# Kernel tuning notes

Measured on AMD Instinct MI355X. Metric: run time of the kernel, lower is better.

## Reference

```python
import jax, jax.numpy as jnp
import numpy as np

N_NODES = 100000
N_EDGES = 1600000
IN_CH, HID_CH, OUT_CH = 256, 128, 64


def setup_inputs() -> dict:
    key = jax.random.key(0)
    k_x, k_e, k1, k2, kb1, kb2 = jax.random.split(key, 6)
    x = jax.random.normal(k_x, (N_NODES, IN_CH), dtype=jnp.float32)
    edge_index = jax.random.randint(k_e, (2, N_EDGES), 0, N_NODES, dtype=jnp.int64)
    # Glorot-style init for GCN linear weights
    W1 = jax.random.normal(k1, (IN_CH, HID_CH), dtype=jnp.float32) * (1.0 / np.sqrt(IN_CH))
    b1 = jnp.zeros((HID_CH,), dtype=jnp.float32)
    W2 = jax.random.normal(k2, (HID_CH, OUT_CH), dtype=jnp.float32) * (1.0 / np.sqrt(HID_CH))
    b2 = jnp.zeros((OUT_CH,), dtype=jnp.float32)
    return {"x": x, "edge_index": edge_index, "W1": W1, "b1": b1, "W2": W2, "b2": b2}


def _gcn_norm(edge_index, n_nodes):
    # add self loops, compute D^{-1/2} (A+I) D^{-1/2} edge weights (PyG gcn_norm)
    loop = jnp.arange(n_nodes, dtype=edge_index.dtype)
    src = jnp.concatenate([edge_index[0], loop])
    dst = jnp.concatenate([edge_index[1], loop])
    deg = jax.ops.segment_sum(jnp.ones_like(src, dtype=jnp.float32), dst, num_segments=n_nodes)
    dinv = jnp.where(deg > 0, jax.lax.rsqrt(jnp.maximum(deg, 1.0)), 0.0)
    norm = dinv[src] * dinv[dst]  # [E + N]
    return src, dst, norm


def _gcn_conv(x, W, b, src, dst, norm, n_nodes):
    h = x @ W                         # linear first (PyG GCNConv)
    msg = norm[:, None] * h[src]      # gather + normalize  [E+N, out]
    agg = jax.ops.segment_sum(msg, dst, num_segments=n_nodes)
    return agg + b


def reference(x, edge_index, W1, b1, W2, b2):
    n = x.shape[0]
    src, dst, norm = _gcn_norm(edge_index, n)
    h = jax.nn.relu(_gcn_conv(x, W1, b1, src, dst, norm, n))
    # dropout is identity in eval mode
    z = _gcn_conv(h, W2, b2, src, dst, norm, n)
    # inner-product decoder on the provided edges, with sigmoid
    e_src, e_dst = edge_index[0], edge_index[1]
    logits = jnp.sum(z[e_src] * z[e_dst], axis=-1)
    return jax.nn.sigmoid(logits)
```

## Files before the change

### kernel.cpp

```cpp
#include <hip/hip_runtime.h>
#include <math.h>

#define N_NODES 100000
#define N_EDGES 1600000
#define IN_CH 256
#define HID_CH 128
#define OUT_CH 64
#define NTILES ((N_NODES + 63) / 64)
#define NB 1024
#define NPART 256
#define EPB (N_EDGES / NPART)
#define NB_USED ((N_NODES + 127) / 128)

typedef short s16x8 __attribute__((ext_vector_type(8)));
typedef unsigned short u16x8 __attribute__((ext_vector_type(8)));
typedef float f32x4 __attribute__((ext_vector_type(4)));

__device__ __forceinline__ float bf2f(unsigned short u) {
    union { unsigned int i; float f; } v;
    v.i = ((unsigned int)u) << 16;
    return v.f;
}
__device__ __forceinline__ unsigned short f2bf(float f) {
    union { float f; unsigned int i; } v;
    v.f = f;
    unsigned int u = v.i;
    return (unsigned short)((u + 0x7FFFu + ((u >> 16) & 1u)) >> 16);
}


__global__ __launch_bounds__(256) void k_hist(const int* __restrict__ dst,
                                              int* __restrict__ ghist) {
    __shared__ int h[NB];
    int b = blockIdx.x, t = threadIdx.x;
    for (int k = t; k < NB; k += 256) h[k] = 0;
    __syncthreads();
    int e0 = b * EPB;
    for (int e = e0 + t; e < e0 + EPB; e += 256)
        atomicAdd(&h[dst[e] >> 7], 1);
    __syncthreads();
    for (int k = t; k < NB; k += 256) ghist[k * NPART + b] = h[k];
}

__global__ __launch_bounds__(256) void k_scan_cols(const int* __restrict__ ghist,
                                                   int* __restrict__ goff,
                                                   int* __restrict__ btot) {
    __shared__ int tmp[NPART];
    int k = blockIdx.x, t = threadIdx.x;
    int v = ghist[k * NPART + t];
    tmp[t] = v;
    __syncthreads();
    for (int off = 1; off < NPART; off <<= 1) {
        int u = (t >= off) ? tmp[t - off] : 0;
        __syncthreads();
        tmp[t] += u;
        __syncthreads();
    }
    goff[k * NPART + t] = tmp[t] - v;
    if (t == NPART - 1) btot[k] = tmp[t];
}

__global__ __launch_bounds__(1024) void k_scan_base(const int* __restrict__ btot,
                                                    int* __restrict__ bbase) {
    __shared__ int tmp[NB];
    int t = threadIdx.x;
    int v = btot[t];
    tmp[t] = v;
    __syncthreads();
    for (int off = 1; off < NB; off <<= 1) {
        int u = (t >= off) ? tmp[t - off] : 0;
        __syncthreads();
        tmp[t] += u;
        __syncthreads();
    }
    bbase[t] = tmp[t] - v;
    if (t == NB - 1) bbase[NB] = tmp[t];
}

__global__ __launch_bounds__(256) void k_partition(const int* __restrict__ src,
                                                   const int* __restrict__ dst,
                                                   const int* __restrict__ goff,
                                                   const int* __restrict__ bbase,
                                                   int2* __restrict__ bsorted) {
    __shared__ int cur[NB];
    int b = blockIdx.x, t = threadIdx.x;
    for (int k = t; k < NB; k += 256) cur[k] = bbase[k] + goff[k * NPART + b];
    __syncthreads();
    int e0 = b * EPB;
    for (int e = e0 + t; e < e0 + EPB; e += 256) {
        int s = src[e], d = dst[e];
        int pos = atomicAdd(&cur[d >> 7], 1);
        bsorted[pos] = make_int2(s, d);
    }
}

__global__ __launch_bounds__(256) void k_bucket_csr(const int2* __restrict__ bsorted,
                                                    const int* __restrict__ bbase,
                                                    int* __restrict__ rowoff,
                                                    float* __restrict__ dinv,
                                                    int* __restrict__ csr_src) {
    __shared__ int cnt[128];
    __shared__ int tmp[256];
    __shared__ int cur[128];
    int b = blockIdx.x, t = threadIdx.x;
    int ebeg = bbase[b], eend = bbase[b + 1];
    if (t < 128) cnt[t] = 0;
    __syncthreads();
    for (int e = ebeg + t; e < eend; e += 256)
        atomicAdd(&cnt[bsorted[e].y & 127], 1);
    __syncthreads();
    int v = (t < 128) ? cnt[t] : 0;
    tmp[t] = v;
    __syncthreads();
    for (int off = 1; off < 256; off <<= 1) {
        int u = (t >= off) ? tmp[t - off] : 0;
        __syncthreads();
        tmp[t] += u;
        __syncthreads();
    }
    if (t < 128) {
        int base = ebeg + tmp[t] - v;
        cur[t] = base;
        int node = b * 128 + t;
        if (node < N_NODES) {
            rowoff[node] = base;
            dinv[node] = rsqrtf((float)v + 1.0f);
        }
    }
    __syncthreads();
    for (int e = ebeg + t; e < eend; e += 256) {
        int2 ed = bsorted[e];
        int pos = atomicAdd(&cur[ed.y & 127], 1);
        csr_src[pos] = ed.x;
    }
}

__global__ __launch_bounds__(256) void k_cast(const float* __restrict__ x,
                                              unsigned short* __restrict__ xb) {
    const int total = N_NODES * IN_CH / 8;
    int stride = gridDim.x * 256;
    for (int i = blockIdx.x * 256 + threadIdx.x; i < total; i += stride) {
        f32x4 a = *reinterpret_cast<const f32x4*>(x + (size_t)i * 8);
        f32x4 b = *reinterpret_cast<const f32x4*>(x + (size_t)i * 8 + 4);
        u16x8 o;
        o[0] = f2bf(a[0]); o[1] = f2bf(a[1]); o[2] = f2bf(a[2]); o[3] = f2bf(a[3]);
        o[4] = f2bf(b[0]); o[5] = f2bf(b[1]); o[6] = f2bf(b[2]); o[7] = f2bf(b[3]);
        *reinterpret_cast<u16x8*>(xb + (size_t)i * 8) = o;
    }
}

__global__ void k_wt1(const float* __restrict__ W1, unsigned short* __restrict__ Wf1) {
    int u = blockIdx.x * 256 + threadIdx.x;
    int f = u >> 6, lane = u & 63;
    int kk = f >> 3, nt = f & 7;
    int l15 = lane & 15, lhi = lane >> 4;
    int n = nt * 16 + l15;
    int kbase = kk * 32 + lhi * 8;
    #pragma unroll
    for (int j = 0; j < 8; ++j)
        Wf1[(size_t)u * 8 + j] = f2bf(W1[(size_t)(kbase + j) * HID_CH + n]);
}

__global__ void k_wt2(const float* __restrict__ W2, unsigned short* __restrict__ Wf2) {
    int u = blockIdx.x * 256 + threadIdx.x;
    int f = u >> 6, lane = u & 63;
    int kk = f >> 2, nt = f & 3;
    int l15 = lane & 15, lhi = lane >> 4;
    int n = nt * 16 + l15;
    int kbase = kk * 32 + lhi * 8;
    #pragma unroll
    for (int j = 0; j < 8; ++j)
        Wf2[(size_t)u * 8 + j] = f2bf(W2[(size_t)(kbase + j) * OUT_CH + n]);
}

__global__ __launch_bounds__(256, 4) void k_gemm1(const unsigned short* __restrict__ xb,
                                                  const unsigned short* __restrict__ Wf1,
                                                  const float* __restrict__ dinv,
                                                  unsigned short* __restrict__ hs1) {
    int tid = threadIdx.x;
    int w = tid >> 6;
    int lane = tid & 63;
    int l15 = lane & 15;
    int lhi = lane >> 4;
    int m0 = blockIdx.x * 64;

    int arow = m0 + w * 16 + l15;
    int arowc = (arow < N_NODES) ? arow : (N_NODES - 1);
    const s16x8* ap = reinterpret_cast<const s16x8*>(xb + (size_t)arowc * IN_CH) + lhi;

    s16x8 af[8];
    #pragma unroll
    for (int kk = 0; kk < 8; ++kk) af[kk] = ap[kk * 4];

    const s16x8* wp = reinterpret_cast<const s16x8*>(Wf1) + lane;

    f32x4 acc[8] = {};
    #pragma unroll
    for (int kk = 0; kk < 8; ++kk) {
        #pragma unroll
        for (int nt = 0; nt < 8; ++nt) {
            s16x8 bf = wp[(kk * 8 + nt) * 64];
            acc[nt] = __builtin_amdgcn_mfma_f32_16x16x32_bf16(af[kk], bf, acc[nt], 0, 0, 0);
        }
    }

    float dv[4];
    int rb = m0 + w * 16 + lhi * 4;
    #pragma unroll
    for (int r = 0; r < 4; ++r) dv[r] = (rb + r < N_NODES) ? dinv[rb + r] : 0.0f;
    #pragma unroll
    for (int nt = 0; nt < 8; ++nt) {
        #pragma unroll
        for (int r = 0; r < 4; ++r) {
            int row = rb + r;
            if (row < N_NODES)
                hs1[(size_t)row * HID_CH + nt * 16 + l15] = f2bf(dv[r] * acc[nt][r]);
        }
    }
}

__global__ __launch_bounds__(256, 4) void k_gemm2(const unsigned short* __restrict__ h1r,
                                                  const unsigned short* __restrict__ Wf2,
                                                  const float* __restrict__ dinv,
                                                  unsigned short* __restrict__ hs2) {
    int tid = threadIdx.x;
    int w = tid >> 6;
    int lane = tid & 63;
    int l15 = lane & 15;
    int lhi = lane >> 4;
    int m0 = blockIdx.x * 64;

    int arow = m0 + w * 16 + l15;
    int arowc = (arow < N_NODES) ? arow : (N_NODES - 1);
    const s16x8* ap = reinterpret_cast<const s16x8*>(h1r + (size_t)arowc * HID_CH) + lhi;

    s16x8 af[4];
    #pragma unroll
    for (int kk = 0; kk < 4; ++kk) af[kk] = ap[kk * 4];

    const s16x8* wp = reinterpret_cast<const s16x8*>(Wf2) + lane;

    f32x4 acc[4] = {};
    #pragma unroll
    for (int kk = 0; kk < 4; ++kk) {
        #pragma unroll
        for (int nt = 0; nt < 4; ++nt) {
            s16x8 bf = wp[(kk * 4 + nt) * 64];
            acc[nt] = __builtin_amdgcn_mfma_f32_16x16x32_bf16(af[kk], bf, acc[nt], 0, 0, 0);
        }
    }

    float dv[4];
    int rb = m0 + w * 16 + lhi * 4;
    #pragma unroll
    for (int r = 0; r < 4; ++r) dv[r] = (rb + r < N_NODES) ? dinv[rb + r] : 0.0f;
    #pragma unroll
    for (int nt = 0; nt < 4; ++nt) {
        #pragma unroll
        for (int r = 0; r < 4; ++r) {
            int row = rb + r;
            if (row < N_NODES)
                hs2[(size_t)row * OUT_CH + nt * 16 + l15] = f2bf(dv[r] * acc[nt][r]);
        }
    }
}

template <int C, bool RELU>
__global__ __launch_bounds__(256) void k_gather_agg(const int* __restrict__ rowoff,
                                                    const int* __restrict__ csr_src,
                                                    const unsigned short* __restrict__ hs,
                                                    const float* __restrict__ dinv,
                                                    const float* __restrict__ b,
                                                    unsigned short* __restrict__ outp) {
    constexpr int TPN = C / 8;
    constexpr int NPB = 256 / TPN;
    int t = threadIdx.x;
    int node = blockIdx.x * NPB + t / TPN;
    int q = t % TPN;
    if (node >= N_NODES) return;

    int beg = rowoff[node];
    int end = (node + 1 < N_NODES) ? rowoff[node + 1] : N_EDGES;

    float acc[8];
    {
        u16x8 sv = *reinterpret_cast<const u16x8*>(&hs[(size_t)node * C + q * 8]);
        #pragma unroll
        for (int j = 0; j < 8; ++j) acc[j] = bf2f(sv[j]);
    }

    int i = beg;
    for (; i + 1 < end; i += 2) {
        int s0 = csr_src[i];
        int s1 = csr_src[i + 1];
        u16x8 v0 = *reinterpret_cast<const u16x8*>(&hs[(size_t)s0 * C + q * 8]);
        u16x8 v1 = *reinterpret_cast<const u16x8*>(&hs[(size_t)s1 * C + q * 8]);
        #pragma unroll
        for (int j = 0; j < 8; ++j) acc[j] += bf2f(v0[j]) + bf2f(v1[j]);
    }
    if (i < end) {
        int s0 = csr_src[i];
        u16x8 v0 = *reinterpret_cast<const u16x8*>(&hs[(size_t)s0 * C + q * 8]);
        #pragma unroll
        for (int j = 0; j < 8; ++j) acc[j] += bf2f(v0[j]);
    }

    float w = dinv[node];
    float4 b0 = reinterpret_cast<const float4*>(b)[q * 2];
    float4 b1 = reinterpret_cast<const float4*>(b)[q * 2 + 1];
    float bb[8] = {b0.x, b0.y, b0.z, b0.w, b1.x, b1.y, b1.z, b1.w};
    u16x8 o;
    #pragma unroll
    for (int j = 0; j < 8; ++j) {
        float v = w * acc[j] + bb[j];
        if (RELU) v = fmaxf(v, 0.0f);
        o[j] = f2bf(v);
    }
    *reinterpret_cast<u16x8*>(&outp[(size_t)node * C + q * 8]) = o;
}


__global__ __launch_bounds__(256) void k_decode(const int* __restrict__ esrc,
                                                const int* __restrict__ edst,
                                                const unsigned short* __restrict__ z,
                                                float* __restrict__ out) {
    int tid = threadIdx.x;
    int e = blockIdx.x * 32 + tid / 8;
    int q = tid % 8;
    if (e >= N_EDGES) return;
    int s = esrc[e], d = edst[e];
    u16x8 a = *reinterpret_cast<const u16x8*>(&z[(size_t)s * OUT_CH + q * 8]);
    u16x8 b = *reinterpret_cast<const u16x8*>(&z[(size_t)d * OUT_CH + q * 8]);
    float dot = 0.0f;
    #pragma unroll
    for (int j = 0; j < 8; ++j) dot += bf2f(a[j]) * bf2f(b[j]);
    dot += __shfl_xor(dot, 1);
    dot += __shfl_xor(dot, 2);
    dot += __shfl_xor(dot, 4);
    if (q == 0) out[e] = 1.0f / (1.0f + expf(-dot));
}


extern "C" void kernel_launch(void* const* d_in, const int* in_sizes, int n_in,
                              void* d_out, int out_size, void* d_ws, size_t ws_size,
                              hipStream_t stream) {
    const float* x  = (const float*)d_in[0];
    const int*   ei = (const int*)d_in[1];
    const float* W1 = (const float*)d_in[2];
    const float* b1 = (const float*)d_in[3];
    const float* W2 = (const float*)d_in[4];
    const float* b2 = (const float*)d_in[5];
    float* out = (float*)d_out;

    const int* src = ei;
    const int* dst = ei + N_EDGES;

    char* ws = (char*)d_ws;
    int*   ghist   = (int*)(ws + 0x000000);
    int*   goff    = (int*)(ws + 0x100000);
    int*   btot    = (int*)(ws + 0x200000);
    int*   bbase   = (int*)(ws + 0x202000);
    int*   rowoff  = (int*)(ws + 0x210000);
    float* dinv    = (float*)(ws + 0x290000);
    unsigned short* Wf1 = (unsigned short*)(ws + 0x310000);
    unsigned short* Wf2 = (unsigned short*)(ws + 0x320000);
    int*   csr_src = (int*)(ws + 0x400000);
    int2*  bsorted = (int2*)(ws + 0xB00000);
    unsigned short* xb  = (unsigned short*)(ws + 0xB00000);
    unsigned short* hs1 = (unsigned short*)(ws + 0x3C00000);
    unsigned short* h1r = (unsigned short*)(ws + 0xB00000);
    unsigned short* hs2 = (unsigned short*)(ws + 0x3C00000);
    unsigned short* z   = (unsigned short*)(ws + 0x2800000);

    k_hist<<<NPART, 256, 0, stream>>>(dst, ghist);
    k_scan_cols<<<NB, 256, 0, stream>>>(ghist, goff, btot);
    k_scan_base<<<1, NB, 0, stream>>>(btot, bbase);
    k_partition<<<NPART, 256, 0, stream>>>(src, dst, goff, bbase, bsorted);
    k_bucket_csr<<<NB_USED, 256, 0, stream>>>(bsorted, bbase, rowoff, dinv, csr_src);

    k_cast<<<2048, 256, 0, stream>>>(x, xb);
    k_wt1<<<16, 256, 0, stream>>>(W1, Wf1);
    k_wt2<<<4, 256, 0, stream>>>(W2, Wf2);

    k_gemm1<<<NTILES, 256, 0, stream>>>(xb, Wf1, dinv, hs1);
    k_gather_agg<HID_CH, true><<<(N_NODES * 16 + 255) / 256, 256, 0, stream>>>(
        rowoff, csr_src, hs1, dinv, b1, h1r);

    k_gemm2<<<NTILES, 256, 0, stream>>>(h1r, Wf2, dinv, hs2);
    k_gather_agg<OUT_CH, false><<<(N_NODES * 8 + 255) / 256, 256, 0, stream>>>(
        rowoff, csr_src, hs2, dinv, b2, z);

    k_decode<<<N_EDGES / 32, 256, 0, stream>>>(src, dst, z, out);
}
```

Baseline: 264.3 us.

## Degree-sort nodes within buckets for gather balance and unroll edge loop by four

The CSR build kernel now ranks the 128 nodes of each bucket by in-degree and writes a permutation, which the gather-aggregate kernels use so that nodes with similar degree share a wavefront. This targets lane divergence from uneven edge counts inside a wave. The edge loop is also unrolled from two to four outstanding loads to raise memory-level parallelism. Costs are an O(128) rank loop per node in the CSR kernel, an extra indirection load, and scattered output writes. Padding nodes in the last bucket map to indices of at least N_NODES and exit early.

```diff
diff --git a/kernel.cpp b/kernel.cpp
--- a/kernel.cpp
+++ b/kernel.cpp
@@ -11,6 +11,7 @@
 #define NPART 256
 #define EPB (N_EDGES / NPART)
 #define NB_USED ((N_NODES + 127) / 128)
+#define NORD (NB_USED * 128)
 
 typedef short s16x8 __attribute__((ext_vector_type(8)));
 typedef unsigned short u16x8 __attribute__((ext_vector_type(8)));
@@ -98,7 +99,8 @@
                                                     const int* __restrict__ bbase,
                                                     int* __restrict__ rowoff,
                                                     float* __restrict__ dinv,
-                                                    int* __restrict__ csr_src) {
+                                                    int* __restrict__ csr_src,
+                                                    int* __restrict__ nodeord) {
     __shared__ int cnt[128];
     __shared__ int tmp[256];
     __shared__ int cur[128];
@@ -126,6 +128,13 @@
             rowoff[node] = base;
             dinv[node] = rsqrtf((float)v + 1.0f);
         }
+        int myd = cnt[t];
+        int rank = 0;
+        for (int j = 0; j < 128; ++j) {
+            int dj = cnt[j];
+            rank += ((dj > myd) || (dj == myd && j < t)) ? 1 : 0;
+        }
+        nodeord[b * 128 + rank] = node;
     }
     __syncthreads();
     for (int e = ebeg + t; e < eend; e += 256) {
@@ -266,7 +275,8 @@
 }
 
 template <int C, bool RELU>
-__global__ __launch_bounds__(256) void k_gather_agg(const int* __restrict__ rowoff,
+__global__ __launch_bounds__(256) void k_gather_agg(const int* __restrict__ nodeord,
+                                                    const int* __restrict__ rowoff,
                                                     const int* __restrict__ csr_src,
                                                     const unsigned short* __restrict__ hs,
                                                     const float* __restrict__ dinv,
@@ -275,7 +285,7 @@
     constexpr int TPN = C / 8;
     constexpr int NPB = 256 / TPN;
     int t = threadIdx.x;
-    int node = blockIdx.x * NPB + t / TPN;
+    int node = nodeord[blockIdx.x * NPB + t / TPN];
     int q = t % TPN;
     if (node >= N_NODES) return;
 
@@ -290,15 +300,17 @@
     }
 
     int i = beg;
-    for (; i + 1 < end; i += 2) {
-        int s0 = csr_src[i];
-        int s1 = csr_src[i + 1];
+    for (; i + 3 < end; i += 4) {
+        int s0 = csr_src[i], s1 = csr_src[i + 1], s2 = csr_src[i + 2], s3 = csr_src[i + 3];
         u16x8 v0 = *reinterpret_cast<const u16x8*>(&hs[(size_t)s0 * C + q * 8]);
         u16x8 v1 = *reinterpret_cast<const u16x8*>(&hs[(size_t)s1 * C + q * 8]);
-        #pragma unroll
-        for (int j = 0; j < 8; ++j) acc[j] += bf2f(v0[j]) + bf2f(v1[j]);
-    }
-    if (i < end) {
+        u16x8 v2 = *reinterpret_cast<const u16x8*>(&hs[(size_t)s2 * C + q * 8]);
+        u16x8 v3 = *reinterpret_cast<const u16x8*>(&hs[(size_t)s3 * C + q * 8]);
+        #pragma unroll
+        for (int j = 0; j < 8; ++j)
+            acc[j] += (bf2f(v0[j]) + bf2f(v1[j])) + (bf2f(v2[j]) + bf2f(v3[j]));
+    }
+    for (; i < end; ++i) {
         int s0 = csr_src[i];
         u16x8 v0 = *reinterpret_cast<const u16x8*>(&hs[(size_t)s0 * C + q * 8]);
         #pragma unroll
@@ -364,6 +376,7 @@
     float* dinv    = (float*)(ws + 0x290000);
     unsigned short* Wf1 = (unsigned short*)(ws + 0x310000);
     unsigned short* Wf2 = (unsigned short*)(ws + 0x320000);
+    int*   nodeord = (int*)(ws + 0x330000);
     int*   csr_src = (int*)(ws + 0x400000);
     int2*  bsorted = (int2*)(ws + 0xB00000);
     unsigned short* xb  = (unsigned short*)(ws + 0xB00000);
@@ -376,19 +389,19 @@
     k_scan_cols<<<NB, 256, 0, stream>>>(ghist, goff, btot);
     k_scan_base<<<1, NB, 0, stream>>>(btot, bbase);
     k_partition<<<NPART, 256, 0, stream>>>(src, dst, goff, bbase, bsorted);
-    k_bucket_csr<<<NB_USED, 256, 0, stream>>>(bsorted, bbase, rowoff, dinv, csr_src);
+    k_bucket_csr<<<NB_USED, 256, 0, stream>>>(bsorted, bbase, rowoff, dinv, csr_src, nodeord);
 
     k_cast<<<2048, 256, 0, stream>>>(x, xb);
     k_wt1<<<16, 256, 0, stream>>>(W1, Wf1);
     k_wt2<<<4, 256, 0, stream>>>(W2, Wf2);
 
     k_gemm1<<<NTILES, 256, 0, stream>>>(xb, Wf1, dinv, hs1);
-    k_gather_agg<HID_CH, true><<<(N_NODES * 16 + 255) / 256, 256, 0, stream>>>(
-        rowoff, csr_src, hs1, dinv, b1, h1r);
+    k_gather_agg<HID_CH, true><<<NORD / 16, 256, 0, stream>>>(
+        nodeord, rowoff, csr_src, hs1, dinv, b1, h1r);
 
     k_gemm2<<<NTILES, 256, 0, stream>>>(h1r, Wf2, dinv, hs2);
-    k_gather_agg<OUT_CH, false><<<(N_NODES * 8 + 255) / 256, 256, 0, stream>>>(
-        rowoff, csr_src, hs2, dinv, b2, z);
+    k_gather_agg<OUT_CH, false><<<NORD / 32, 256, 0, stream>>>(
+        nodeord, rowoff, csr_src, hs2, dinv, b2, z);
 
     k_decode<<<N_EDGES / 32, 256, 0, stream>>>(src, dst, z, out);
 }
```

After: 281.6 us. +6.5%, slower.
